# Performance work log

Measured on AMD Instinct MI355X. Metric: run time of the kernel, lower is better.

## Reference

```python
import jax, jax.numpy as jnp
import numpy as np

B, CIN, COUT, H, W = 16, 64, 64, 128, 128
MH, MW = 32, 32  # retained Fourier modes


def setup_inputs() -> dict:
    key = jax.random.key(0)
    k1, k2, k3 = jax.random.split(key, 3)
    scale = 1.0 / (CIN * COUT)  # 'auto' scale in the torch module
    x = jax.random.normal(k1, (B, CIN, H, W), dtype=jnp.float32)
    # packed complex weight: dim0 = (real, imag), dim1 = corner (top=0, bottom=1)
    weight = scale * jax.random.normal(k2, (2, 2, CIN, COUT, MH, MW), dtype=jnp.float32)
    bias = scale * jax.random.normal(k3, (COUT, 1, 1), dtype=jnp.float32)
    return {"x": x, "weight": weight, "bias": bias, "super_res": 1}


def reference(x, weight, bias, super_res):
    b, ci, h, w = x.shape
    # rfft2 over the last two spatial dims (norm='backward' is default)
    xf = jnp.fft.rfft2(x.astype(jnp.float32), norm="backward")  # [b, ci, h, w//2+1] c64
    wc = (weight[0] + 1j * weight[1]).astype(jnp.complex64)  # [2, ci, co, mh, mw]
    # low-frequency corner contractions: bixy,ioxy->boxy
    top = jnp.einsum("bixy,ioxy->boxy", xf[:, :, :MH, :MW], wc[0])
    bot = jnp.einsum("bixy,ioxy->boxy", xf[:, :, h - MH:, :MW], wc[1])
    out_fft = jnp.zeros((b, COUT, h, w // 2 + 1), dtype=jnp.complex64)
    out_fft = out_fft.at[:, :, :MH, :MW:super_res].set(top)
    out_fft = out_fft.at[:, :, h - MH:, :MW:super_res].set(bot)
    out_size = (int(h * super_res), int(w * super_res))
    y = jnp.fft.irfft2(out_fft, s=out_size, norm="backward").astype(x.dtype)
    return y + bias  # bias [co,1,1] broadcasts over spatial dims
```

## Files before the change

kernel.cpp:

```cpp
#include <hip/hip_runtime.h>


__device__ __forceinline__ void build_tab(float* tabs) {
    int t = threadIdx.x;
    if (t < 128) {
        float ang = (float)t * 0.049087385212340517f;
        float s, c;
        sincosf(ang, &s, &c);
        tabs[t] = c;
        tabs[129 + t] = s;
    }
}

__global__ __launch_bounds__(256) void kAB(const float* __restrict__ x,
                                           float* __restrict__ XF) {
    __shared__ float tabs[258];
    __shared__ __align__(16) float smem[8704];
    build_tab(tabs);
    __syncthreads();
    int t = threadIdx.x;
    size_t bc = blockIdx.x;
    float* Twid = smem;
    float* xeo  = smem + 4096;
    #pragma unroll
    for (int i = 0; i < 16; ++i) {
        int e = t + i * 256;
        int w = e >> 6, q = e & 63, kx = q >> 1;
        int idx = (w * kx) & 127;
        Twid[e] = (q & 1) ? -tabs[129 + idx] : tabs[idx];
    }
    const float* xb = x + bc * 16384;
    int th = t & 31;
    int tq = t >> 5;
    int q0 = tq * 8;
    int wl4 = (t & 3) * 4;
    int hb  = t >> 2;
    float4 rlo0, rhi0, rlo1, rhi1;
    auto loadR = [&](int ph) {
        rlo0 = *(const float4*)(xb + hb * 128 + ph * 16 + wl4);
        rhi0 = *(const float4*)(xb + hb * 128 + ph * 16 + wl4 + 64);
        rlo1 = *(const float4*)(xb + (64 + hb) * 128 + ph * 16 + wl4);
        rhi1 = *(const float4*)(xb + (64 + hb) * 128 + ph * 16 + wl4 + 64);
    };
    auto writeR = [&]() {
        int h0 = hb, h1 = 64 + hb;
        *(float2*)(&xeo[(wl4+0)*260 + 2*h0]) = make_float2(rlo0.x+rhi0.x, rlo0.x-rhi0.x);
        *(float2*)(&xeo[(wl4+1)*260 + 2*h0]) = make_float2(rlo0.y+rhi0.y, rlo0.y-rhi0.y);
        *(float2*)(&xeo[(wl4+2)*260 + 2*h0]) = make_float2(rlo0.z+rhi0.z, rlo0.z-rhi0.z);
        *(float2*)(&xeo[(wl4+3)*260 + 2*h0]) = make_float2(rlo0.w+rhi0.w, rlo0.w-rhi0.w);
        *(float2*)(&xeo[(wl4+0)*260 + 2*h1]) = make_float2(rlo1.x+rhi1.x, rlo1.x-rhi1.x);
        *(float2*)(&xeo[(wl4+1)*260 + 2*h1]) = make_float2(rlo1.y+rhi1.y, rlo1.y-rhi1.y);
        *(float2*)(&xeo[(wl4+2)*260 + 2*h1]) = make_float2(rlo1.z+rhi1.z, rlo1.z-rhi1.z);
        *(float2*)(&xeo[(wl4+3)*260 + 2*h1]) = make_float2(rlo1.w+rhi1.w, rlo1.w-rhi1.w);
    };
    loadR(0);
    writeR();
    float4 acc[8];
    #pragma unroll
    for (int j = 0; j < 8; ++j) acc[j] = make_float4(0.f, 0.f, 0.f, 0.f);
    __syncthreads();
    for (int ph = 0; ph < 4; ++ph) {
        if (ph < 3) loadR(ph + 1);
        #pragma unroll 4
        for (int wl = 0; wl < 16; ++wl) {
            int w = ph * 16 + wl;
            const float* xr = &xeo[wl * 260 + 4 * th];
            float4 d0  = *(const float4*)(xr);
            float4 d1  = *(const float4*)(xr + 128);
            float4 tw0 = *(const float4*)(&Twid[w * 64 + q0]);
            float4 tw1 = *(const float4*)(&Twid[w * 64 + q0 + 4]);
            acc[0].x = fmaf(d0.x, tw0.x, acc[0].x); acc[0].y = fmaf(d0.x, tw0.y, acc[0].y);
            acc[0].z = fmaf(d0.y, tw0.z, acc[0].z); acc[0].w = fmaf(d0.y, tw0.w, acc[0].w);
            acc[1].x = fmaf(d0.x, tw1.x, acc[1].x); acc[1].y = fmaf(d0.x, tw1.y, acc[1].y);
            acc[1].z = fmaf(d0.y, tw1.z, acc[1].z); acc[1].w = fmaf(d0.y, tw1.w, acc[1].w);
            acc[2].x = fmaf(d0.z, tw0.x, acc[2].x); acc[2].y = fmaf(d0.z, tw0.y, acc[2].y);
            acc[2].z = fmaf(d0.w, tw0.z, acc[2].z); acc[2].w = fmaf(d0.w, tw0.w, acc[2].w);
            acc[3].x = fmaf(d0.z, tw1.x, acc[3].x); acc[3].y = fmaf(d0.z, tw1.y, acc[3].y);
            acc[3].z = fmaf(d0.w, tw1.z, acc[3].z); acc[3].w = fmaf(d0.w, tw1.w, acc[3].w);
            acc[4].x = fmaf(d1.x, tw0.x, acc[4].x); acc[4].y = fmaf(d1.x, tw0.y, acc[4].y);
            acc[4].z = fmaf(d1.y, tw0.z, acc[4].z); acc[4].w = fmaf(d1.y, tw0.w, acc[4].w);
            acc[5].x = fmaf(d1.x, tw1.x, acc[5].x); acc[5].y = fmaf(d1.x, tw1.y, acc[5].y);
            acc[5].z = fmaf(d1.y, tw1.z, acc[5].z); acc[5].w = fmaf(d1.y, tw1.w, acc[5].w);
            acc[6].x = fmaf(d1.z, tw0.x, acc[6].x); acc[6].y = fmaf(d1.z, tw0.y, acc[6].y);
            acc[6].z = fmaf(d1.w, tw0.z, acc[6].z); acc[6].w = fmaf(d1.w, tw0.w, acc[6].w);
            acc[7].x = fmaf(d1.z, tw1.x, acc[7].x); acc[7].y = fmaf(d1.z, tw1.y, acc[7].y);
            acc[7].z = fmaf(d1.w, tw1.z, acc[7].z); acc[7].w = fmaf(d1.w, tw1.w, acc[7].w);
        }
        __syncthreads();
        if (ph < 3) {
            writeR();
            __syncthreads();
        }
    }
    float* Af = smem;
    {
        int base = th * 68 + q0;
        *(float4*)(&Af[base])          = make_float4(acc[0].x+acc[4].x, acc[0].y+acc[4].y, acc[0].z+acc[4].z, acc[0].w+acc[4].w);
        *(float4*)(&Af[base + 4])      = make_float4(acc[1].x+acc[5].x, acc[1].y+acc[5].y, acc[1].z+acc[5].z, acc[1].w+acc[5].w);
        *(float4*)(&Af[2176 + base])   = make_float4(acc[0].x-acc[4].x, acc[0].y-acc[4].y, acc[0].z-acc[4].z, acc[0].w-acc[4].w);
        *(float4*)(&Af[2176 + base+4]) = make_float4(acc[1].x-acc[5].x, acc[1].y-acc[5].y, acc[1].z-acc[5].z, acc[1].w-acc[5].w);
        *(float4*)(&Af[4352 + base])   = make_float4(acc[2].x+acc[6].x, acc[2].y+acc[6].y, acc[2].z+acc[6].z, acc[2].w+acc[6].w);
        *(float4*)(&Af[4352 + base+4]) = make_float4(acc[3].x+acc[7].x, acc[3].y+acc[7].y, acc[3].z+acc[7].z, acc[3].w+acc[7].w);
        *(float4*)(&Af[6528 + base])   = make_float4(acc[2].x-acc[6].x, acc[2].y-acc[6].y, acc[2].z-acc[6].z, acc[2].w-acc[6].w);
        *(float4*)(&Af[6528 + base+4]) = make_float4(acc[3].x-acc[7].x, acc[3].y-acc[7].y, acc[3].z-acc[7].z, acc[3].w-acc[7].w);
    }
    __syncthreads();
    {
        int k = t & 31, kxg = t >> 5;
        int kx0 = kxg * 4;
        int sig = k & 1;
        const float* pe = Af + sig * 2176;
        const float* po = Af + 4352 + sig * 2176;
        int a2 = (2 * k) & 127;
        float ca = tabs[a2], sa = tabs[129 + a2];
        float ce = 1.f, se = 0.f;
        float co_ = tabs[k], so_ = tabs[129 + k];
        float4 P1 = {0,0,0,0}, P2 = {0,0,0,0}, P3 = {0,0,0,0}, P4 = {0,0,0,0};
        for (int m = 0; m < 32; ++m) {
            float4 ae01 = *(const float4*)(pe + m * 68 + 2 * kx0);
            float4 ae23 = *(const float4*)(pe + m * 68 + 2 * kx0 + 4);
            float4 ao01 = *(const float4*)(po + m * 68 + 2 * kx0);
            float4 ao23 = *(const float4*)(po + m * 68 + 2 * kx0 + 4);
            P1.x = fmaf(ae01.x, ce, P1.x); P1.x = fmaf(ao01.x, co_, P1.x);
            P2.x = fmaf(ae01.y, se, P2.x); P2.x = fmaf(ao01.y, so_, P2.x);
            P3.x = fmaf(ae01.y, ce, P3.x); P3.x = fmaf(ao01.y, co_, P3.x);
            P4.x = fmaf(ae01.x, se, P4.x); P4.x = fmaf(ao01.x, so_, P4.x);
            P1.y = fmaf(ae01.z, ce, P1.y); P1.y = fmaf(ao01.z, co_, P1.y);
            P2.y = fmaf(ae01.w, se, P2.y); P2.y = fmaf(ao01.w, so_, P2.y);
            P3.y = fmaf(ae01.w, ce, P3.y); P3.y = fmaf(ao01.w, co_, P3.y);
            P4.y = fmaf(ae01.z, se, P4.y); P4.y = fmaf(ao01.z, so_, P4.y);
            P1.z = fmaf(ae23.x, ce, P1.z); P1.z = fmaf(ao23.x, co_, P1.z);
            P2.z = fmaf(ae23.y, se, P2.z); P2.z = fmaf(ao23.y, so_, P2.z);
            P3.z = fmaf(ae23.y, ce, P3.z); P3.z = fmaf(ao23.y, co_, P3.z);
            P4.z = fmaf(ae23.x, se, P4.z); P4.z = fmaf(ao23.x, so_, P4.z);
            P1.w = fmaf(ae23.z, ce, P1.w); P1.w = fmaf(ao23.z, co_, P1.w);
            P2.w = fmaf(ae23.w, se, P2.w); P2.w = fmaf(ao23.w, so_, P2.w);
            P3.w = fmaf(ae23.w, ce, P3.w); P3.w = fmaf(ao23.w, co_, P3.w);
            P4.w = fmaf(ae23.z, se, P4.w); P4.w = fmaf(ao23.z, so_, P4.w);
            float t1 = se * sa, t2 = ce * sa;
            float cen = fmaf(ce, ca, -t1);
            float sen = fmaf(se, ca, t2);
            ce = cen; se = sen;
            float t3 = so_ * sa, t4 = co_ * sa;
            float con = fmaf(co_, ca, -t3);
            float son = fmaf(so_, ca, t4);
            co_ = con; so_ = son;
        }
        float* xfb = XF + bc * 4096;
        *(float4*)(xfb + (k * 32 + kx0) * 2) =
            make_float4(P1.x + P2.x, P3.x - P4.x, P1.y + P2.y, P3.y - P4.y);
        *(float4*)(xfb + (k * 32 + kx0) * 2 + 4) =
            make_float4(P1.z + P2.z, P3.z - P4.z, P1.w + P2.w, P3.w - P4.w);
        if (k) {
            *(float4*)(xfb + ((64 - k) * 32 + kx0) * 2) =
                make_float4(P1.x - P2.x, P3.x + P4.x, P1.y - P2.y, P3.y + P4.y);
            *(float4*)(xfb + ((64 - k) * 32 + kx0) * 2 + 4) =
                make_float4(P1.z - P2.z, P3.z + P4.z, P1.w - P2.w, P3.w + P4.w);
        }
        if (t < 32) {
            int kx = t;
            float re = 0.f, im = 0.f;
            #pragma unroll 8
            for (int m = 0; m < 32; ++m) {
                float2 aep = *(const float2*)(&Af[       m * 68 + 2 * kx]);
                float2 aop = *(const float2*)(&Af[4352 + m * 68 + 2 * kx]);
                float sg = (m & 1) ? -1.f : 1.f;
                re = fmaf(sg, aep.x - aop.y, re);
                im = fmaf(sg, aep.y + aop.x, im);
            }
            xfb[(32 * 32 + kx) * 2]     = re;
            xfb[(32 * 32 + kx) * 2 + 1] = im;
        }
    }
}

__global__ __launch_bounds__(256, 4) void kC(const float* __restrict__ XF,
                                             const float* __restrict__ Wgt,
                                             float* __restrict__ YF0,
                                             float* __restrict__ YF1) {
    __shared__ float2 Xs[2048];
    int t = threadIdx.x;
    int bid = blockIdx.x;
    int cih = bid & 1;
    int mxh = (bid >> 1) & 1;
    int cot = (bid >> 2) & 7;
    int my  = (bid >> 5) & 31;
    int c   = bid >> 10;
    int co0 = cot * 8;
    int slotbase = (c * 32 + my) * 32 + mxh * 16;
    int mx   = t & 15;
    int co_l = (t >> 4) & 7;
    int bh   = t >> 7;
    int co = co0 + co_l;
    int ci0 = cih * 32;
    float2 acc[8];
    #pragma unroll
    for (int i = 0; i < 8; ++i) acc[i] = make_float2(0.f, 0.f);
    const float* wp = Wgt + (size_t)c * 4194304 + (size_t)my * 32 + mxh * 16 + mx
                          + ((size_t)(ci0 * 64) + co) * 1024;
    float2 rwA[8], rwB[8], rx[8];
    auto loadW = [&](int cc, float2* rw) {
        #pragma unroll
        for (int j = 0; j < 8; ++j) {
            size_t off = (size_t)(cc * 8 + j) * 65536;
            rw[j].x = wp[off];
            rw[j].y = wp[off + 8388608];
        }
    };
    auto loadX = [&](int cc) {
        #pragma unroll
        for (int s = 0; s < 8; ++s) {
            int e = t + s * 256;
            int emx = e & 15, eb = (e >> 4) & 15, eci = e >> 8;
            int ci = ci0 + cc * 8 + eci;
            rx[s] = *(const float2*)(XF + ((size_t)(eb * 64 + ci) * 2048 + slotbase + emx) * 2);
        }
    };
    auto writeX = [&]() {
        #pragma unroll
        for (int s = 0; s < 8; ++s) Xs[t + s * 256] = rx[s];
    };
#define KC_COMPUTE(RW)                                                       \
    {                                                                        \
        _Pragma("unroll")                                                    \
        for (int j = 0; j < 8; ++j) {                                        \
            float2 w = RW[j];                                                \
            _Pragma("unroll")                                                \
            for (int bb = 0; bb < 8; ++bb) {                                 \
                float2 xv = Xs[(j * 16 + bh * 8 + bb) * 16 + mx];            \
                acc[bb].x = fmaf(xv.x, w.x, acc[bb].x);                      \
                acc[bb].x = fmaf(-xv.y, w.y, acc[bb].x);                     \
                acc[bb].y = fmaf(xv.x, w.y, acc[bb].y);                      \
                acc[bb].y = fmaf(xv.y, w.x, acc[bb].y);                      \
            }                                                                \
        }                                                                    \
    }
    loadX(0); loadW(0, rwA); loadW(1, rwB);
    writeX();
    __syncthreads();
    loadX(1);
    KC_COMPUTE(rwA);
    loadW(2, rwA);
    __syncthreads();
    writeX(); __syncthreads();
    loadX(2);
    KC_COMPUTE(rwB);
    loadW(3, rwB);
    __syncthreads();
    writeX(); __syncthreads();
    loadX(3);
    KC_COMPUTE(rwA);
    __syncthreads();
    writeX(); __syncthreads();
    KC_COMPUTE(rwB);
#undef KC_COMPUTE
    float* YF = cih ? YF1 : YF0;
    #pragma unroll
    for (int bb = 0; bb < 8; ++bb) {
        int b = bh * 8 + bb;
        *(float2*)(YF + ((size_t)(b * 64 + co) * 2048 + slotbase + mx) * 2) = acc[bb];
    }
}

__global__ __launch_bounds__(256) void kDE(const float* __restrict__ YF0,
                                           const float* __restrict__ YF1,
                                           const float* __restrict__ bias,
                                           float* __restrict__ out) {
    __shared__ float tabs[258];
    __shared__ __align__(16) float Ts[4096];
    __shared__ __align__(16) float U[8448];
    build_tab(tabs);
    __syncthreads();
    int t = threadIdx.x;
    size_t bo = blockIdx.x;
    const float inv = 6.103515625e-05f;
    #pragma unroll
    for (int i = 0; i < 16; ++i) {
        int e = t + i * 256;
        int q = e >> 6, w = e & 63;
        int k = q >> 1;
        int idx = (k * w) & 127;
        float val;
        if (q == 0)      val = inv;
        else if (q == 1) val = 0.f;
        else if (q & 1)  val = -2.f * inv * tabs[129 + idx];
        else             val =  2.f * inv * tabs[idx];
        Ts[e] = val;
    }
    float* Qs = U;
    float* Rs = U + 2112;
    const float* y0 = YF0 + bo * 4096;
    const float* y1 = YF1 + bo * 4096;
    for (int u = t; u < 528; u += 256) {
        int k = u >> 4, kxf = (u & 15) * 4;
        float4 a0 = *(const float4*)(y0 + k * 64 + kxf);
        float4 a1 = *(const float4*)(y1 + k * 64 + kxf);
        float4 a = make_float4(a0.x+a1.x, a0.y+a1.y, a0.z+a1.z, a0.w+a1.w);
        float4 Q, R;
        if (k == 0) { Q = a; R = make_float4(0.f, 0.f, 0.f, 0.f); }
        else if (k == 32) { Q = a; R = make_float4(-a.x, -a.y, -a.z, -a.w); }
        else {
            float4 b0 = *(const float4*)(y0 + (64 - k) * 64 + kxf);
            float4 b1 = *(const float4*)(y1 + (64 - k) * 64 + kxf);
            float4 bb = make_float4(b0.x+b1.x, b0.y+b1.y, b0.z+b1.z, b0.w+b1.w);
            Q = make_float4(a.x+bb.x, a.y+bb.y, a.z+bb.z, a.w+bb.w);
            R = make_float4(a.x-bb.x, a.y-bb.y, a.z-bb.z, a.w-bb.w);
        }
        *(float4*)(&Qs[k * 64 + kxf]) = Q;
        *(float4*)(&Rs[k * 64 + kxf]) = R;
    }
    __syncthreads();
    int hh = t >> 2;
    int kx0 = (t & 3) * 8;
    float4 Ee0 = {0,0,0,0}, Ee1 = {0,0,0,0}, Ee2 = {0,0,0,0}, Ee3 = {0,0,0,0};
    float4 Eo0 = {0,0,0,0}, Eo1 = {0,0,0,0}, Eo2 = {0,0,0,0}, Eo3 = {0,0,0,0};
    int idx = 0;
#define KD_BODY(E0, E1, E2, E3, kk)                                          \
    {                                                                        \
        float c = tabs[idx], s = tabs[129 + idx];                            \
        const float4* Qp = (const float4*)(&Qs[(kk) * 64 + kx0 * 2]);        \
        const float4* Rp = (const float4*)(&Rs[(kk) * 64 + kx0 * 2]);        \
        float4 Qv, Rv;                                                       \
        Qv = Qp[0]; Rv = Rp[0];                                              \
        E0.x = fmaf(c, Qv.x, E0.x); E0.x = fmaf(-s, Rv.y, E0.x);             \
        E0.y = fmaf(c, Qv.y, E0.y); E0.y = fmaf(s, Rv.x, E0.y);              \
        E0.z = fmaf(c, Qv.z, E0.z); E0.z = fmaf(-s, Rv.w, E0.z);             \
        E0.w = fmaf(c, Qv.w, E0.w); E0.w = fmaf(s, Rv.z, E0.w);              \
        Qv = Qp[1]; Rv = Rp[1];                                              \
        E1.x = fmaf(c, Qv.x, E1.x); E1.x = fmaf(-s, Rv.y, E1.x);             \
        E1.y = fmaf(c, Qv.y, E1.y); E1.y = fmaf(s, Rv.x, E1.y);              \
        E1.z = fmaf(c, Qv.z, E1.z); E1.z = fmaf(-s, Rv.w, E1.z);             \
        E1.w = fmaf(c, Qv.w, E1.w); E1.w = fmaf(s, Rv.z, E1.w);              \
        Qv = Qp[2]; Rv = Rp[2];                                              \
        E2.x = fmaf(c, Qv.x, E2.x); E2.x = fmaf(-s, Rv.y, E2.x);             \
        E2.y = fmaf(c, Qv.y, E2.y); E2.y = fmaf(s, Rv.x, E2.y);              \
        E2.z = fmaf(c, Qv.z, E2.z); E2.z = fmaf(-s, Rv.w, E2.z);             \
        E2.w = fmaf(c, Qv.w, E2.w); E2.w = fmaf(s, Rv.z, E2.w);              \
        Qv = Qp[3]; Rv = Rp[3];                                              \
        E3.x = fmaf(c, Qv.x, E3.x); E3.x = fmaf(-s, Rv.y, E3.x);             \
        E3.y = fmaf(c, Qv.y, E3.y); E3.y = fmaf(s, Rv.x, E3.y);              \
        E3.z = fmaf(c, Qv.z, E3.z); E3.z = fmaf(-s, Rv.w, E3.z);             \
        E3.w = fmaf(c, Qv.w, E3.w); E3.w = fmaf(s, Rv.z, E3.w);              \
        idx = (idx + hh) & 127;                                              \
    }
    for (int u = 0; u < 16; ++u) {
        KD_BODY(Ee0, Ee1, Ee2, Ee3, 2 * u);
        KD_BODY(Eo0, Eo1, Eo2, Eo3, 2 * u + 1);
    }
    KD_BODY(Ee0, Ee1, Ee2, Ee3, 32);
#undef KD_BODY
    __syncthreads();
    float* Zt = U;
    {
        float* zr = &Zt[(2 * kx0) * 132 + hh];
        float* zs = zr + 64;
        zr[0*132]  = Ee0.x + Eo0.x;  zs[0*132]  = Ee0.x - Eo0.x;
        zr[1*132]  = Ee0.y + Eo0.y;  zs[1*132]  = Ee0.y - Eo0.y;
        zr[2*132]  = Ee0.z + Eo0.z;  zs[2*132]  = Ee0.z - Eo0.z;
        zr[3*132]  = Ee0.w + Eo0.w;  zs[3*132]  = Ee0.w - Eo0.w;
        zr[4*132]  = Ee1.x + Eo1.x;  zs[4*132]  = Ee1.x - Eo1.x;
        zr[5*132]  = Ee1.y + Eo1.y;  zs[5*132]  = Ee1.y - Eo1.y;
        zr[6*132]  = Ee1.z + Eo1.z;  zs[6*132]  = Ee1.z - Eo1.z;
        zr[7*132]  = Ee1.w + Eo1.w;  zs[7*132]  = Ee1.w - Eo1.w;
        zr[8*132]  = Ee2.x + Eo2.x;  zs[8*132]  = Ee2.x - Eo2.x;
        zr[9*132]  = Ee2.y + Eo2.y;  zs[9*132]  = Ee2.y - Eo2.y;
        zr[10*132] = Ee2.z + Eo2.z;  zs[10*132] = Ee2.z - Eo2.z;
        zr[11*132] = Ee2.w + Eo2.w;  zs[11*132] = Ee2.w - Eo2.w;
        zr[12*132] = Ee3.x + Eo3.x;  zs[12*132] = Ee3.x - Eo3.x;
        zr[13*132] = Ee3.y + Eo3.y;  zs[13*132] = Ee3.y - Eo3.y;
        zr[14*132] = Ee3.z + Eo3.z;  zs[14*132] = Ee3.z - Eo3.z;
        zr[15*132] = Ee3.w + Eo3.w;  zs[15*132] = Ee3.w - Eo3.w;
    }
    __syncthreads();
    int w0 = (t & 31) * 2;
    int h0 = (t >> 5) * 16;
    float2 We[16], Wo[16];
    #pragma unroll
    for (int j = 0; j < 16; ++j) { We[j] = make_float2(0.f, 0.f); Wo[j] = make_float2(0.f, 0.f); }
#define KE_K(E, K)                                                            \
    {                                                                         \
        const float4* zpe = (const float4*)(&Zt[(2*(K)) * 132 + h0]);         \
        const float4* zpo = (const float4*)(&Zt[(2*(K)+1) * 132 + h0]);       \
        float2 twe = *(const float2*)(&Ts[(2*(K)) * 64 + w0]);                \
        float2 two = *(const float2*)(&Ts[(2*(K)+1) * 64 + w0]);              \
        float4 e0 = zpe[0], e1 = zpe[1], e2 = zpe[2], e3 = zpe[3];            \
        float4 o0 = zpo[0], o1 = zpo[1], o2 = zpo[2], o3 = zpo[3];            \
        E[0].x  = fmaf(e0.x, twe.x, E[0].x);  E[0].x  = fmaf(o0.x, two.x, E[0].x);   \
        E[0].y  = fmaf(e0.x, twe.y, E[0].y);  E[0].y  = fmaf(o0.x, two.y, E[0].y);   \
        E[1].x  = fmaf(e0.y, twe.x, E[1].x);  E[1].x  = fmaf(o0.y, two.x, E[1].x);   \
        E[1].y  = fmaf(e0.y, twe.y, E[1].y);  E[1].y  = fmaf(o0.y, two.y, E[1].y);   \
        E[2].x  = fmaf(e0.z, twe.x, E[2].x);  E[2].x  = fmaf(o0.z, two.x, E[2].x);   \
        E[2].y  = fmaf(e0.z, twe.y, E[2].y);  E[2].y  = fmaf(o0.z, two.y, E[2].y);   \
        E[3].x  = fmaf(e0.w, twe.x, E[3].x);  E[3].x  = fmaf(o0.w, two.x, E[3].x);   \
        E[3].y  = fmaf(e0.w, twe.y, E[3].y);  E[3].y  = fmaf(o0.w, two.y, E[3].y);   \
        E[4].x  = fmaf(e1.x, twe.x, E[4].x);  E[4].x  = fmaf(o1.x, two.x, E[4].x);   \
        E[4].y  = fmaf(e1.x, twe.y, E[4].y);  E[4].y  = fmaf(o1.x, two.y, E[4].y);   \
        E[5].x  = fmaf(e1.y, twe.x, E[5].x);  E[5].x  = fmaf(o1.y, two.x, E[5].x);   \
        E[5].y  = fmaf(e1.y, twe.y, E[5].y);  E[5].y  = fmaf(o1.y, two.y, E[5].y);   \
        E[6].x  = fmaf(e1.z, twe.x, E[6].x);  E[6].x  = fmaf(o1.z, two.x, E[6].x);   \
        E[6].y  = fmaf(e1.z, twe.y, E[6].y);  E[6].y  = fmaf(o1.z, two.y, E[6].y);   \
        E[7].x  = fmaf(e1.w, twe.x, E[7].x);  E[7].x  = fmaf(o1.w, two.x, E[7].x);   \
        E[7].y  = fmaf(e1.w, twe.y, E[7].y);  E[7].y  = fmaf(o1.w, two.y, E[7].y);   \
        E[8].x  = fmaf(e2.x, twe.x, E[8].x);  E[8].x  = fmaf(o2.x, two.x, E[8].x);   \
        E[8].y  = fmaf(e2.x, twe.y, E[8].y);  E[8].y  = fmaf(o2.x, two.y, E[8].y);   \
        E[9].x  = fmaf(e2.y, twe.x, E[9].x);  E[9].x  = fmaf(o2.y, two.x, E[9].x);   \
        E[9].y  = fmaf(e2.y, twe.y, E[9].y);  E[9].y  = fmaf(o2.y, two.y, E[9].y);   \
        E[10].x = fmaf(e2.z, twe.x, E[10].x); E[10].x = fmaf(o2.z, two.x, E[10].x);  \
        E[10].y = fmaf(e2.z, twe.y, E[10].y); E[10].y = fmaf(o2.z, two.y, E[10].y);  \
        E[11].x = fmaf(e2.w, twe.x, E[11].x); E[11].x = fmaf(o2.w, two.x, E[11].x);  \
        E[11].y = fmaf(e2.w, twe.y, E[11].y); E[11].y = fmaf(o2.w, two.y, E[11].y);  \
        E[12].x = fmaf(e3.x, twe.x, E[12].x); E[12].x = fmaf(o3.x, two.x, E[12].x);  \
        E[12].y = fmaf(e3.x, twe.y, E[12].y); E[12].y = fmaf(o3.x, two.y, E[12].y);  \
        E[13].x = fmaf(e3.y, twe.x, E[13].x); E[13].x = fmaf(o3.y, two.x, E[13].x);  \
        E[13].y = fmaf(e3.y, twe.y, E[13].y); E[13].y = fmaf(o3.y, two.y, E[13].y);  \
        E[14].x = fmaf(e3.z, twe.x, E[14].x); E[14].x = fmaf(o3.z, two.x, E[14].x);  \
        E[14].y = fmaf(e3.z, twe.y, E[14].y); E[14].y = fmaf(o3.z, two.y, E[14].y);  \
        E[15].x = fmaf(e3.w, twe.x, E[15].x); E[15].x = fmaf(o3.w, two.x, E[15].x);  \
        E[15].y = fmaf(e3.w, twe.y, E[15].y); E[15].y = fmaf(o3.w, two.y, E[15].y);  \
    }
    #pragma unroll 2
    for (int u = 0; u < 16; ++u) {
        KE_K(We, 2 * u);
        KE_K(Wo, 2 * u + 1);
    }
#undef KE_K
    float bv = bias[(int)(bo & 63)];
    float* ob = out + ((size_t)(bo * 128 + h0)) * 128;
    #pragma unroll
    for (int j = 0; j < 16; ++j) {
        float2 lo = make_float2(We[j].x + Wo[j].x + bv, We[j].y + Wo[j].y + bv);
        float2 hi = make_float2(We[j].x - Wo[j].x + bv, We[j].y - Wo[j].y + bv);
        *(float2*)(ob + (size_t)j * 128 + w0)      = lo;
        *(float2*)(ob + (size_t)j * 128 + w0 + 64) = hi;
    }
}

extern "C" void kernel_launch(void* const* d_in, const int* in_sizes, int n_in,
                              void* d_out, int out_size, void* d_ws, size_t ws_size,
                              hipStream_t stream) {
    (void)in_sizes; (void)n_in; (void)out_size; (void)ws_size;
    const float* x    = (const float*)d_in[0];
    const float* wgt  = (const float*)d_in[1];
    const float* bias = (const float*)d_in[2];
    float* outp   = (float*)d_out;
    char* ws = (char*)d_ws;
    float* bufXF  = (float*)(ws + (48u << 20));
    float* bufYF0 = (float*)(ws);
    float* bufYF1 = (float*)(ws + (16u << 20));
    hipLaunchKernelGGL(kAB, dim3(1024), dim3(256), 0, stream, x, bufXF);
    hipLaunchKernelGGL(kC, dim3(2048), dim3(256), 0, stream, bufXF, wgt, bufYF0, bufYF1);
    hipLaunchKernelGGL(kDE, dim3(1024), dim3(256), 0, stream, bufYF0, bufYF1, bias, outp);
}
```

Measured before the change: 117.1 us.

## Stage kC inputs and weights into LDS via direct global-to-LDS loads, double-buffered

The spectral-contraction kernel now copies both the Fourier input tile and the complex weight tile straight from global memory into shared memory with the 16-byte global_load_lds builtin. It uses two shared buffers so the load of the next ci chunk overlaps compute on the current one. Previously weights were loaded per thread into registers with scalar loads, and inputs went through registers before being written to LDS. The aim is fewer register staging copies and wider, coalesced loads. The cost is more LDS per block, the removal of the occupancy hint from launch bounds, and reliance on the barrier placement to order the asynchronous LDS writes.

```diff
diff --git a/kernel.cpp b/kernel.cpp
--- a/kernel.cpp
+++ b/kernel.cpp
@@ -174,12 +174,14 @@
     }
 }
 
-__global__ __launch_bounds__(256, 4) void kC(const float* __restrict__ XF,
-                                             const float* __restrict__ Wgt,
-                                             float* __restrict__ YF0,
-                                             float* __restrict__ YF1) {
-    __shared__ float2 Xs[2048];
+__global__ __launch_bounds__(256) void kC(const float* __restrict__ XF,
+                                          const float* __restrict__ Wgt,
+                                          float* __restrict__ YF0,
+                                          float* __restrict__ YF1) {
+    __shared__ __align__(16) float2 Xb[2][2048];
+    __shared__ __align__(16) float  Wb[2][2048];
     int t = threadIdx.x;
+    int lane = t & 63, wid = t >> 6;
     int bid = blockIdx.x;
     int cih = bid & 1;
     int mxh = (bid >> 1) & 1;
@@ -196,63 +198,58 @@
     float2 acc[8];
     #pragma unroll
     for (int i = 0; i < 8; ++i) acc[i] = make_float2(0.f, 0.f);
-    const float* wp = Wgt + (size_t)c * 4194304 + (size_t)my * 32 + mxh * 16 + mx
-                          + ((size_t)(ci0 * 64) + co) * 1024;
-    float2 rwA[8], rwB[8], rx[8];
-    auto loadW = [&](int cc, float2* rw) {
+    const float* wbase = Wgt + (size_t)c * 4194304 + (size_t)my * 32 + mxh * 16;
+    auto stage = [&](int cc, int buf) {
         #pragma unroll
-        for (int j = 0; j < 8; ++j) {
-            size_t off = (size_t)(cc * 8 + j) * 65536;
-            rw[j].x = wp[off];
-            rw[j].y = wp[off + 8388608];
+        for (int i = 0; i < 4; ++i) {
+            int inst = wid * 4 + i;
+            int u = inst * 64 + lane;
+            int mxp = u & 7, b = (u >> 3) & 15, ci_l = u >> 7;
+            int ci = ci0 + cc * 8 + ci_l;
+            const float* g = XF + ((size_t)(b * 64 + ci) * 2048 + slotbase + mxp * 2) * 2;
+            float* l = (float*)Xb[buf] + inst * 256;
+            __builtin_amdgcn_global_load_lds(g, l, 16, 0, 0);
+        }
+        #pragma unroll
+        for (int i = 0; i < 2; ++i) {
+            int inst = wid * 2 + i;
+            int u = inst * 64 + lane;
+            int mx4 = u & 3, col = (u >> 2) & 7, ci_l = (u >> 5) & 7, pl = u >> 8;
+            const float* g = wbase + (size_t)pl * 8388608
+                           + ((size_t)(ci0 + cc * 8 + ci_l) * 64 + co0 + col) * 1024
+                           + mx4 * 4;
+            float* l = Wb[buf] + inst * 256;
+            __builtin_amdgcn_global_load_lds(g, l, 16, 0, 0);
         }
     };
-    auto loadX = [&](int cc) {
-        #pragma unroll
-        for (int s = 0; s < 8; ++s) {
-            int e = t + s * 256;
-            int emx = e & 15, eb = (e >> 4) & 15, eci = e >> 8;
-            int ci = ci0 + cc * 8 + eci;
-            rx[s] = *(const float2*)(XF + ((size_t)(eb * 64 + ci) * 2048 + slotbase + emx) * 2);
-        }
-    };
-    auto writeX = [&]() {
-        #pragma unroll
-        for (int s = 0; s < 8; ++s) Xs[t + s * 256] = rx[s];
-    };
-#define KC_COMPUTE(RW)                                                       \
+#define KC_COMPUTE(BUF)                                                      \
     {                                                                        \
         _Pragma("unroll")                                                    \
         for (int j = 0; j < 8; ++j) {                                        \
-            float2 w = RW[j];                                                \
+            float wre = Wb[BUF][(j * 8 + co_l) * 16 + mx];                   \
+            float wim = Wb[BUF][1024 + (j * 8 + co_l) * 16 + mx];            \
             _Pragma("unroll")                                                \
             for (int bb = 0; bb < 8; ++bb) {                                 \
-                float2 xv = Xs[(j * 16 + bh * 8 + bb) * 16 + mx];            \
-                acc[bb].x = fmaf(xv.x, w.x, acc[bb].x);                      \
-                acc[bb].x = fmaf(-xv.y, w.y, acc[bb].x);                     \
-                acc[bb].y = fmaf(xv.x, w.y, acc[bb].y);                      \
-                acc[bb].y = fmaf(xv.y, w.x, acc[bb].y);                      \
+                float2 xv = Xb[BUF][(j * 16 + bh * 8 + bb) * 16 + mx];       \
+                acc[bb].x = fmaf(xv.x, wre, acc[bb].x);                      \
+                acc[bb].x = fmaf(-xv.y, wim, acc[bb].x);                     \
+                acc[bb].y = fmaf(xv.x, wim, acc[bb].y);                      \
+                acc[bb].y = fmaf(xv.y, wre, acc[bb].y);                      \
             }                                                                \
         }                                                                    \
     }
-    loadX(0); loadW(0, rwA); loadW(1, rwB);
-    writeX();
-    __syncthreads();
-    loadX(1);
-    KC_COMPUTE(rwA);
-    loadW(2, rwA);
-    __syncthreads();
-    writeX(); __syncthreads();
-    loadX(2);
-    KC_COMPUTE(rwB);
-    loadW(3, rwB);
-    __syncthreads();
-    writeX(); __syncthreads();
-    loadX(3);
-    KC_COMPUTE(rwA);
-    __syncthreads();
-    writeX(); __syncthreads();
-    KC_COMPUTE(rwB);
+    stage(0, 0);
+    __syncthreads();
+    stage(1, 1);
+    KC_COMPUTE(0);
+    __syncthreads();
+    stage(2, 0);
+    KC_COMPUTE(1);
+    __syncthreads();
+    stage(3, 1);
+    KC_COMPUTE(0);
+    __syncthreads();
+    KC_COMPUTE(1);
 #undef KC_COMPUTE
     float* YF = cih ? YF1 : YF0;
     #pragma unroll
```

New measurement: 117.5 us. About the same (+0.3%).
